# Optimization experiments

Hardware: AMD Instinct MI355X
Metric: run time of the kernel (lower is better)

## Reference

```python
import jax
import jax.numpy as jnp
import numpy as np

B, R, C, Q, D = 16, 2048, 81, 65, 1024
K = 1024          # pre-NMS candidate cap (fixed-shape stand-in for torch's dynamic filtering)
DET = 100         # detections_per_img
IMG = 640.0       # square image size (clip bound)
SCORE_THRESH = 0.05
NMS_THRESH = 0.5
MIN_SIZE = 0.01
BBOX_CLIP = float(np.log(1000.0 / 16.0))  # torchvision BoxCoder bbox_xform_clip
WX, WY, WW, WH = 10.0, 10.0, 5.0, 5.0     # BoxCoder weights


def setup_inputs() -> dict:
    key = jax.random.key(0)
    k1, k2, k3, k4, k5, k6 = jax.random.split(key, 6)
    class_logits = 2.0 * jax.random.normal(k1, (B, R, C), jnp.float32)
    quantity_logits = jax.random.normal(k2, (B, R, Q), jnp.float32)
    box_features = jax.random.normal(k3, (B, R, D), jnp.float32)
    box_regression = 0.5 * jax.random.normal(k4, (B, R, C * 4), jnp.float32)
    cxcy = jax.random.uniform(k5, (B, R, 2), jnp.float32, 0.0, IMG)
    wh = jax.random.uniform(k6, (B, R, 2), jnp.float32, 10.0, 80.0)
    x1y1 = jnp.clip(cxcy - 0.5 * wh, 0.0, IMG)
    x2y2 = jnp.clip(cxcy + 0.5 * wh, 0.0, IMG)
    proposals = jnp.concatenate([x1y1, x2y2], axis=-1)
    return {
        'class_logits': class_logits,
        'quantity_logits': quantity_logits,
        'box_features': box_features,
        'box_regression': box_regression,
        'proposals': proposals,
    }


def _decode(deltas, props):
    # deltas: [R, C, 4], props: [R, 4] -> boxes [R, C, 4] (torchvision BoxCoder.decode)
    pw = props[:, 2] - props[:, 0]
    ph = props[:, 3] - props[:, 1]
    pcx = props[:, 0] + 0.5 * pw
    pcy = props[:, 1] + 0.5 * ph
    dx = deltas[..., 0] / WX
    dy = deltas[..., 1] / WY
    dw = jnp.minimum(deltas[..., 2] / WW, BBOX_CLIP)
    dh = jnp.minimum(deltas[..., 3] / WH, BBOX_CLIP)
    cx = dx * pw[:, None] + pcx[:, None]
    cy = dy * ph[:, None] + pcy[:, None]
    w = jnp.exp(dw) * pw[:, None]
    h = jnp.exp(dh) * ph[:, None]
    return jnp.stack([cx - 0.5 * w, cy - 0.5 * h, cx + 0.5 * w, cy + 0.5 * h], axis=-1)


def _iou_matrix(b):
    # b: [K, 4] -> pairwise IoU [K, K]
    area = (b[:, 2] - b[:, 0]) * (b[:, 3] - b[:, 1])
    lt = jnp.maximum(b[:, None, :2], b[None, :, :2])
    rb = jnp.minimum(b[:, None, 2:], b[None, :, 2:])
    whv = jnp.clip(rb - lt, 0.0)
    inter = whv[..., 0] * whv[..., 1]
    return inter / (area[:, None] + area[None, :] - inter + 1e-9)


def _process_image(logits, qlogits, feats, reg, props):
    # decode + clip
    boxes = jnp.clip(_decode(reg.reshape(R, C, 4), props), 0.0, IMG)  # [R, C, 4]
    scores = jax.nn.softmax(logits, axis=-1)                          # [R, C]
    quant = jnp.argmax(qlogits, axis=-1).astype(jnp.int32)            # [R]
    # drop background class 0, flatten to M = R*(C-1)
    fb = boxes[:, 1:, :].reshape(-1, 4)
    fs = scores[:, 1:].reshape(-1)
    fl = jnp.broadcast_to(jnp.arange(1, C, dtype=jnp.int32), (R, C - 1)).reshape(-1)
    fi = jnp.broadcast_to(jnp.arange(R, dtype=jnp.int32)[:, None], (R, C - 1)).reshape(-1)
    bw = fb[:, 2] - fb[:, 0]
    bh = fb[:, 3] - fb[:, 1]
    valid = (fs > SCORE_THRESH) & (bw >= MIN_SIZE) & (bh >= MIN_SIZE)
    # top-K candidates by masked score (sorted desc)
    top_s, top_i = jax.lax.top_k(jnp.where(valid, fs, -1.0), K)
    cb = fb[top_i]          # [K, 4]
    cl = fl[top_i]          # [K]
    ci = fi[top_i]          # [K] row index into proposals/features
    cv = top_s > 0.0        # candidate validity (score_thresh > 0)
    # batched NMS via per-class coordinate offset
    ob = cb + (cl.astype(jnp.float32) * (IMG + 1.0))[:, None]
    iou = _iou_matrix(ob)
    ar = jnp.arange(K)

    def body(i, keep):
        sup = (iou[i] > NMS_THRESH) & (ar > i)
        return jnp.where(keep[i] & cv[i], keep & ~sup, keep)

    keep = jax.lax.fori_loop(0, K, body, cv) & cv
    # first DET survivors in score order
    det_s, det_i = jax.lax.top_k(jnp.where(keep, top_s, -1.0), DET)
    dv = det_s > 0.0
    m = dv.astype(jnp.float32)
    db = cb[det_i] * m[:, None]
    dl = jnp.where(dv, cl[det_i], 0)
    di = ci[det_i]
    dq = jnp.where(dv, quant[di], 0)
    df = feats[di] * m[:, None]   # irregular gather of box features by surviving row idx
    ds = jnp.where(dv, det_s, 0.0)
    return db, ds, dl, dq, df, dv


def reference(class_logits, quantity_logits, box_features, box_regression, proposals):
    # returns (boxes [B,DET,4], scores [B,DET], labels [B,DET] i32,
    #          quantities [B,DET] i32, features [B,DET,D], valid [B,DET] bool)
    return jax.vmap(_process_image)(class_logits, quantity_logits, box_features,
                                    box_regression, proposals)
```

## Files before the change

### kernel.cpp

```cpp
#include <hip/hip_runtime.h>
#include <math.h>

#define NB 16
#define NR 2048
#define NC 81
#define NQ 65
#define ND 1024
#define NK 1024
#define NDET 100
#define NBLK 512
#define BSLOT 64
#define HBINS 5184
#define BBC 4.135166556742356f

#define O_BOX   0
#define O_SCORE (NB*NDET*4)
#define O_LABEL (O_SCORE + NB*NDET)
#define O_QUANT (O_LABEL + NB*NDET)
#define O_FEAT  (O_QUANT + NB*NDET)
#define O_VALID (O_FEAT + (size_t)NB*NDET*ND)

#define WS_CAND  ((size_t)0)
#define WS_CNT   (WS_CAND + (size_t)NB*NBLK*BSLOT*8)
#define WS_QUANT (WS_CNT + (size_t)NB*NBLK*4)
#define WS_SELM  (WS_QUANT + (size_t)NB*NR*4)
#define WS_SELS  (WS_SELM + (size_t)NB*NK*4)
#define WS_CB    (WS_SELS + (size_t)NB*NK*4)
#define WS_DETK  (WS_CB + (size_t)NB*NK*16)

__device__ __forceinline__ float4 decode_box(float4 d, float pw, float ph,
                                             float pcx, float pcy) {
    float dx = d.x / 10.0f, dy = d.y / 10.0f;
    float dw = fminf(d.z / 5.0f, BBC), dh = fminf(d.w / 5.0f, BBC);
    float cx = dx * pw + pcx, cy = dy * ph + pcy;
    float w = expf(dw) * pw, h = expf(dh) * ph;
    float4 r;
    r.x = fminf(fmaxf(cx - 0.5f * w, 0.0f), 640.0f);
    r.y = fminf(fmaxf(cy - 0.5f * h, 0.0f), 640.0f);
    r.z = fminf(fmaxf(cx + 0.5f * w, 0.0f), 640.0f);
    r.w = fminf(fmaxf(cy + 0.5f * h, 0.0f), 640.0f);
    return r;
}

__global__ __launch_bounds__(256) void k_stage1(
    const float* __restrict__ logits, const float* __restrict__ qlog,
    const float* __restrict__ reg, const float* __restrict__ props,
    unsigned long long* __restrict__ cand, int* __restrict__ cnt,
    int* __restrict__ quant) {
    __shared__ unsigned long long sl[BSLOT];
    __shared__ int scnt;
    int b = blockIdx.x >> 9;
    int blk = blockIdx.x & (NBLK - 1);
    int wid = threadIdx.x >> 6;
    int lane = threadIdx.x & 63;
    int r = blk * 4 + wid;
    int row = b * NR + r;
    if (threadIdx.x == 0) scnt = 0;
    __syncthreads();

    const float* Lrow = logits + (size_t)row * NC;
    float v0 = Lrow[lane];
    float v1 = (lane < NC - 64) ? Lrow[64 + lane] : -1e30f;
    float mx = fmaxf(v0, v1);
    #pragma unroll
    for (int o = 32; o; o >>= 1) mx = fmaxf(mx, __shfl_xor(mx, o));
    float e = expf(v0 - mx) + ((lane < NC - 64) ? expf(v1 - mx) : 0.0f);
    float sm = e;
    #pragma unroll
    for (int o = 32; o; o >>= 1) sm += __shfl_xor(sm, o);
    float thr_lo = mx + logf(0.05f * sm) - 0.01f;

    const float* Qrow = qlog + (size_t)row * NQ;
    float qv = Qrow[lane];
    int qi = lane;
    if (lane == 0) {
        float q64 = Qrow[64];
        if (q64 > qv) { qv = q64; qi = 64; }
    }
    #pragma unroll
    for (int o = 32; o; o >>= 1) {
        float ov = __shfl_xor(qv, o);
        int oi = __shfl_xor(qi, o);
        if (ov > qv || (ov == qv && oi < qi)) { qv = ov; qi = oi; }
    }
    if (lane == 0) quant[row] = qi;

    const float* P = props + (size_t)row * 4;
    float p0 = P[0], p1 = P[1], p2 = P[2], p3 = P[3];
    float pw = p2 - p0, ph = p3 - p1;
    float pcx = p0 + 0.5f * pw, pcy = p1 + 0.5f * ph;
    const float* G = reg + (size_t)row * (NC * 4);

    #pragma unroll
    for (int pass = 0; pass < 2; ++pass) {
        int cc = lane + pass * 64;
        if (cc < NC - 1) {
            int c = cc + 1;
            float lc = Lrow[c];
            if (lc > thr_lo) {
                float p = expf(lc - mx) / sm;
                float4 d = *(const float4*)(G + 4 * c);
                float4 bx = decode_box(d, pw, ph, pcx, pcy);
                float bw = bx.z - bx.x, bh = bx.w - bx.y;
                if (p > 0.05f && bw >= 0.01f && bh >= 0.01f) {
                    int m = r * 80 + cc;
                    int pos = atomicAdd(&scnt, 1);
                    if (pos < BSLOT)
                        sl[pos] = ((unsigned long long)__float_as_uint(p) << 32) |
                                  (unsigned)(~(unsigned)m);
                }
            }
        }
    }
    __syncthreads();
    int n = scnt < BSLOT ? scnt : BSLOT;
    unsigned long long* dst = cand + ((size_t)b * NBLK + blk) * BSLOT;
    for (int i = threadIdx.x; i < n; i += 256) dst[i] = sl[i];
    if (threadIdx.x == 0) cnt[b * NBLK + blk] = n;
}

__global__ __launch_bounds__(1024) void k_fused(
    const unsigned long long* __restrict__ cand, const int* __restrict__ cnt,
    const float* __restrict__ reg, const float* __restrict__ props,
    int* __restrict__ sel_m, float* __restrict__ sel_s,
    float4* __restrict__ cb, int* __restrict__ det_k) {
    __shared__ unsigned int hist[HBINS];
    __shared__ unsigned long long list[2048];
    __shared__ float4 boxes[NK];
    __shared__ int scn[NBLK];
    __shared__ int s_cnt, s_bstar, s_n;
    int b = blockIdx.x, tid = threadIdx.x;
    const unsigned long long* cnd = cand + (size_t)b * NBLK * BSLOT;

    for (int i = tid; i < HBINS; i += 1024) hist[i] = 0;
    if (tid < NBLK) scn[tid] = cnt[b * NBLK + tid];
    if (tid == 0) { s_cnt = 0; s_bstar = 0; }
    __syncthreads();

    for (int i = tid; i < NBLK * BSLOT; i += 1024) {
        if ((i & (BSLOT - 1)) < scn[i >> 6]) {
            unsigned bits = (unsigned)(cnd[i] >> 32);
            atomicAdd(&hist[(bits - 0x3D000000u) >> 13], 1u);
        }
    }
    __syncthreads();

    if (tid < 64) {
        int lane = tid, base = lane * 81;
        unsigned partial = 0;
        for (int j = 0; j < 81; ++j) partial += hist[base + j];
        unsigned incl = partial;
        #pragma unroll
        for (int o = 1; o < 64; o <<= 1) {
            unsigned t = __shfl_up(incl, o);
            if (lane >= o) incl += t;
        }
        unsigned total = __shfl(incl, 63);
        unsigned suffix = total - incl;
        if (suffix < NK && suffix + partial >= NK) {
            unsigned A = suffix;
            int bcross = base;
            for (int bb = base + 80; bb >= base; --bb) {
                unsigned An = A + hist[bb];
                if (An >= NK) { bcross = bb; break; }
                A = An;
            }
            s_bstar = bcross;
        }
    }
    __syncthreads();
    int bstar = s_bstar;

    for (int i = tid; i < NBLK * BSLOT; i += 1024) {
        if ((i & (BSLOT - 1)) < scn[i >> 6]) {
            unsigned long long key = cnd[i];
            int bin = (int)(((unsigned)(key >> 32) - 0x3D000000u) >> 13);
            if (bin >= bstar) {
                int p = atomicAdd(&s_cnt, 1);
                if (p < 2048) list[p] = key;
            }
        }
    }
    __syncthreads();
    int S = s_cnt;
    if (S > 2048) S = 2048;
    int n = 2;
    while (n < S) n <<= 1;
    for (int i = S + tid; i < n; i += 1024) list[i] = 0ull;
    __syncthreads();

    for (int k2 = 2; k2 <= n; k2 <<= 1)
        for (int j = k2 >> 1; j > 0; j >>= 1) {
            for (int i = tid; i < n; i += 1024) {
                int ixj = i ^ j;
                if (ixj > i) {
                    unsigned long long a = list[i], c = list[ixj];
                    bool descRegion = ((i & k2) == 0);
                    if ((a < c) == descRegion) { list[i] = c; list[ixj] = a; }
                }
            }
            __syncthreads();
        }

    int L = S < NK ? S : NK;
    if (tid == 0) s_n = L;
    if (tid < L) {
        unsigned long long key = list[tid];
        int m = (int)(~(unsigned)key);
        sel_m[b * NK + tid] = m;
        sel_s[b * NK + tid] = __uint_as_float((unsigned)(key >> 32));
        int r = m / 80, c = m - r * 80 + 1;
        size_t row = (size_t)b * NR + r;
        const float* P = props + row * 4;
        float p0 = P[0], p1 = P[1], p2 = P[2], p3 = P[3];
        float pw = p2 - p0, ph = p3 - p1;
        float pcx = p0 + 0.5f * pw, pcy = p1 + 0.5f * ph;
        float4 d = *(const float4*)(reg + row * (NC * 4) + 4 * c);
        float4 bx = decode_box(d, pw, ph, pcx, pcy);
        cb[(size_t)b * NK + tid] = bx;
        float off = (float)c * 641.0f;
        float4 o = {bx.x + off, bx.y + off, bx.z + off, bx.w + off};
        boxes[tid] = o;
    }
    __syncthreads();

    if (tid < 64) {
        int lane = tid, nn = s_n, A = 0;
        float4 a0 = {0, 0, 0, 0}, a1 = {0, 0, 0, 0};
        int* dk = det_k + b * NDET;
        float4 nxt = (nn > 0) ? boxes[0] : a0;
        for (int t = 0; t < nn && A < NDET; ++t) {
            float4 bt = nxt;
            if (t + 1 < nn) nxt = boxes[t + 1];
            float areaB = (bt.z - bt.x) * (bt.w - bt.y);
            float areaA0 = (a0.z - a0.x) * (a0.w - a0.y);
            float ltx = fmaxf(a0.x, bt.x), lty = fmaxf(a0.y, bt.y);
            float rbx = fminf(a0.z, bt.z), rby = fminf(a0.w, bt.w);
            float inter = fmaxf(rbx - ltx, 0.0f) * fmaxf(rby - lty, 0.0f);
            bool sup = (lane < A) &&
                       (inter / (areaA0 + areaB - inter + 1e-9f) > 0.5f);
            if (A > 64) {
                float areaA1 = (a1.z - a1.x) * (a1.w - a1.y);
                float ltx1 = fmaxf(a1.x, bt.x), lty1 = fmaxf(a1.y, bt.y);
                float rbx1 = fminf(a1.z, bt.z), rby1 = fminf(a1.w, bt.w);
                float in1 = fmaxf(rbx1 - ltx1, 0.0f) * fmaxf(rby1 - lty1, 0.0f);
                sup |= (lane + 64 < A) &&
                       (in1 / (areaA1 + areaB - in1 + 1e-9f) > 0.5f);
            }
            if (!__any((int)sup)) {
                if (lane == (A & 63)) {
                    if (A < 64) a0 = bt; else a1 = bt;
                }
                if (lane == 0) dk[A] = t;
                ++A;
            }
        }
        for (int d = A + lane; d < NDET; d += 64) dk[d] = -1;
    }
}

__global__ __launch_bounds__(256) void k_final(
    const float* __restrict__ feats, const int* __restrict__ quant,
    const int* __restrict__ sel_m, const float* __restrict__ sel_s,
    const float4* __restrict__ cb, const int* __restrict__ det_k,
    float* __restrict__ out) {
    int bd = blockIdx.x;
    int b = bd / NDET, d = bd - b * NDET;
    int t = threadIdx.x;
    int k = det_k[b * NDET + d];
    float4* of = (float4*)(out + O_FEAT + (size_t)bd * ND);
    if (k >= 0) {
        int m = sel_m[b * NK + k];
        int r = m / 80, c = m - r * 80 + 1;
        if (t == 0) {
            ((float4*)(out + O_BOX))[bd] = cb[(size_t)b * NK + k];
            out[O_SCORE + bd] = sel_s[b * NK + k];
            out[O_LABEL + bd] = (float)c;
            out[O_QUANT + bd] = (float)quant[b * NR + r];
            out[O_VALID + bd] = 1.0f;
        }
        const float4* f = (const float4*)(feats + ((size_t)b * NR + r) * ND);
        of[t] = f[t];
    } else {
        if (t == 0) {
            float4 z = {0, 0, 0, 0};
            ((float4*)(out + O_BOX))[bd] = z;
            out[O_SCORE + bd] = 0.0f;
            out[O_LABEL + bd] = 0.0f;
            out[O_QUANT + bd] = 0.0f;
            out[O_VALID + bd] = 0.0f;
        }
        float4 z = {0, 0, 0, 0};
        of[t] = z;
    }
}

extern "C" void kernel_launch(void* const* d_in, const int* in_sizes, int n_in,
                              void* d_out, int out_size, void* d_ws, size_t ws_size,
                              hipStream_t stream) {
    const float* logits = (const float*)d_in[0];
    const float* qlog   = (const float*)d_in[1];
    const float* feats  = (const float*)d_in[2];
    const float* reg    = (const float*)d_in[3];
    const float* props  = (const float*)d_in[4];
    float* out = (float*)d_out;
    char* ws = (char*)d_ws;

    unsigned long long* cand = (unsigned long long*)(ws + WS_CAND);
    int* cnt = (int*)(ws + WS_CNT);
    int* quant = (int*)(ws + WS_QUANT);
    int* sel_m = (int*)(ws + WS_SELM);
    float* sel_s = (float*)(ws + WS_SELS);
    float4* cb = (float4*)(ws + WS_CB);
    int* det_k = (int*)(ws + WS_DETK);

    k_stage1<<<NB * NBLK, 256, 0, stream>>>(logits, qlog, reg, props, cand, cnt,
                                            quant);
    k_fused<<<NB, 1024, 0, stream>>>(cand, cnt, reg, props, sel_m, sel_s, cb,
                                     det_k);
    k_final<<<NB * NDET, 256, 0, stream>>>(feats, quant, sel_m, sel_s, cb, det_k,
                                           out);
}
```

Baseline: 304.7 us.

## Build histogram in stage1, two-tier rank sort, lazy NMS of tail candidates

The score histogram is now built with global atomics in stage1, so the single-block fused kernel no longer makes an extra pass over candidates. The top-1024 bitonic sort is replaced by a two-tier selection: the top ~256 candidates are rank-sorted and run through NMS first. The remaining candidates are only rank-sorted and decoded when fewer than 100 detections survive. The quantity argmax moves from all rows into the final kernel, which runs it only for surviving detections. The trade-offs are a memset plus global atomics, and an O(n^2) rank sort in the fallback path.

```diff
diff --git a/kernel.cpp b/kernel.cpp
--- a/kernel.cpp
+++ b/kernel.cpp
@@ -11,6 +11,9 @@
 #define NBLK 512
 #define BSLOT 64
 #define HBINS 5184
+#define CH 256
+#define L2CAP 384
+#define LRCAP 1536
 #define BBC 4.135166556742356f
 
 #define O_BOX   0
@@ -21,12 +24,11 @@
 #define O_VALID (O_FEAT + (size_t)NB*NDET*ND)
 
 #define WS_CAND  ((size_t)0)
-#define WS_CNT   (WS_CAND + (size_t)NB*NBLK*BSLOT*8)
-#define WS_QUANT (WS_CNT + (size_t)NB*NBLK*4)
-#define WS_SELM  (WS_QUANT + (size_t)NB*NR*4)
-#define WS_SELS  (WS_SELM + (size_t)NB*NK*4)
-#define WS_CB    (WS_SELS + (size_t)NB*NK*4)
-#define WS_DETK  (WS_CB + (size_t)NB*NK*16)
+#define WS_GHIST (WS_CAND + (size_t)NB*NBLK*BSLOT*8)
+#define WS_DETCB (WS_GHIST + (size_t)NB*HBINS*4)
+#define WS_DETM  (WS_DETCB + (size_t)NB*NDET*16)
+#define WS_DETS  (WS_DETM + (size_t)NB*NDET*4)
+#define WS_CNT   (WS_DETS + (size_t)NB*NDET*4)
 
 __device__ __forceinline__ float4 decode_box(float4 d, float pw, float ph,
                                              float pcx, float pcy) {
@@ -43,10 +45,9 @@
 }
 
 __global__ __launch_bounds__(256) void k_stage1(
-    const float* __restrict__ logits, const float* __restrict__ qlog,
-    const float* __restrict__ reg, const float* __restrict__ props,
-    unsigned long long* __restrict__ cand, int* __restrict__ cnt,
-    int* __restrict__ quant) {
+    const float* __restrict__ logits, const float* __restrict__ reg,
+    const float* __restrict__ props, unsigned long long* __restrict__ cand,
+    int* __restrict__ cnt, unsigned int* __restrict__ ghist) {
     __shared__ unsigned long long sl[BSLOT];
     __shared__ int scnt;
     int b = blockIdx.x >> 9;
@@ -69,21 +70,6 @@
     #pragma unroll
     for (int o = 32; o; o >>= 1) sm += __shfl_xor(sm, o);
     float thr_lo = mx + logf(0.05f * sm) - 0.01f;
-
-    const float* Qrow = qlog + (size_t)row * NQ;
-    float qv = Qrow[lane];
-    int qi = lane;
-    if (lane == 0) {
-        float q64 = Qrow[64];
-        if (q64 > qv) { qv = q64; qi = 64; }
-    }
-    #pragma unroll
-    for (int o = 32; o; o >>= 1) {
-        float ov = __shfl_xor(qv, o);
-        int oi = __shfl_xor(qi, o);
-        if (ov > qv || (ov == qv && oi < qi)) { qv = ov; qi = oi; }
-    }
-    if (lane == 0) quant[row] = qi;
 
     const float* P = props + (size_t)row * 4;
     float p0 = P[0], p1 = P[1], p2 = P[2], p3 = P[3];
@@ -105,9 +91,12 @@
                 if (p > 0.05f && bw >= 0.01f && bh >= 0.01f) {
                     int m = r * 80 + cc;
                     int pos = atomicAdd(&scnt, 1);
-                    if (pos < BSLOT)
+                    if (pos < BSLOT) {
                         sl[pos] = ((unsigned long long)__float_as_uint(p) << 32) |
                                   (unsigned)(~(unsigned)m);
+                        unsigned bin = (__float_as_uint(p) - 0x3D000000u) >> 13;
+                        atomicAdd(&ghist[b * HBINS + bin], 1u);
+                    }
                 }
             }
         }
@@ -121,34 +110,31 @@
 
 __global__ __launch_bounds__(1024) void k_fused(
     const unsigned long long* __restrict__ cand, const int* __restrict__ cnt,
+    const unsigned int* __restrict__ ghist,
     const float* __restrict__ reg, const float* __restrict__ props,
-    int* __restrict__ sel_m, float* __restrict__ sel_s,
-    float4* __restrict__ cb, int* __restrict__ det_k) {
-    __shared__ unsigned int hist[HBINS];
-    __shared__ unsigned long long list[2048];
-    __shared__ float4 boxes[NK];
+    int* __restrict__ det_m, float* __restrict__ det_s,
+    float4* __restrict__ det_cb) {
+    __shared__ union {
+        unsigned int hist[HBINS];
+        unsigned long long sortedRest[LRCAP];
+    } u;
+    __shared__ unsigned long long list2[L2CAP], sorted2[L2CAP];
+    __shared__ unsigned long long listRest[LRCAP];
+    __shared__ float4 boff[L2CAP], bclip[L2CAP];
     __shared__ int scn[NBLK];
-    __shared__ int s_cnt, s_bstar, s_n;
+    __shared__ int s_c2, s_cR, s_b1, s_b2, s_A, s_need;
     int b = blockIdx.x, tid = threadIdx.x;
     const unsigned long long* cnd = cand + (size_t)b * NBLK * BSLOT;
 
-    for (int i = tid; i < HBINS; i += 1024) hist[i] = 0;
+    for (int i = tid; i < HBINS; i += 1024) u.hist[i] = ghist[b * HBINS + i];
     if (tid < NBLK) scn[tid] = cnt[b * NBLK + tid];
-    if (tid == 0) { s_cnt = 0; s_bstar = 0; }
-    __syncthreads();
-
-    for (int i = tid; i < NBLK * BSLOT; i += 1024) {
-        if ((i & (BSLOT - 1)) < scn[i >> 6]) {
-            unsigned bits = (unsigned)(cnd[i] >> 32);
-            atomicAdd(&hist[(bits - 0x3D000000u) >> 13], 1u);
-        }
-    }
+    if (tid == 0) { s_c2 = 0; s_cR = 0; s_b1 = 0; s_b2 = 0; s_A = 0; s_need = 0; }
     __syncthreads();
 
     if (tid < 64) {
         int lane = tid, base = lane * 81;
         unsigned partial = 0;
-        for (int j = 0; j < 81; ++j) partial += hist[base + j];
+        for (int j = 0; j < 81; ++j) partial += u.hist[base + j];
         unsigned incl = partial;
         #pragma unroll
         for (int o = 1; o < 64; o <<= 1) {
@@ -159,127 +145,198 @@
         unsigned suffix = total - incl;
         if (suffix < NK && suffix + partial >= NK) {
             unsigned A = suffix;
-            int bcross = base;
             for (int bb = base + 80; bb >= base; --bb) {
-                unsigned An = A + hist[bb];
-                if (An >= NK) { bcross = bb; break; }
+                unsigned An = A + u.hist[bb];
+                if (An >= NK) { s_b1 = bb; break; }
                 A = An;
             }
-            s_bstar = bcross;
-        }
-    }
-    __syncthreads();
-    int bstar = s_bstar;
+        }
+        if (suffix < CH && suffix + partial >= CH) {
+            unsigned A = suffix;
+            for (int bb = base + 80; bb >= base; --bb) {
+                unsigned An = A + u.hist[bb];
+                if (An >= CH) { s_b2 = bb; break; }
+                A = An;
+            }
+        }
+    }
+    __syncthreads();
+    int b1 = s_b1, b2 = s_b2;
 
     for (int i = tid; i < NBLK * BSLOT; i += 1024) {
         if ((i & (BSLOT - 1)) < scn[i >> 6]) {
             unsigned long long key = cnd[i];
             int bin = (int)(((unsigned)(key >> 32) - 0x3D000000u) >> 13);
-            if (bin >= bstar) {
-                int p = atomicAdd(&s_cnt, 1);
-                if (p < 2048) list[p] = key;
-            }
-        }
-    }
-    __syncthreads();
-    int S = s_cnt;
-    if (S > 2048) S = 2048;
-    int n = 2;
-    while (n < S) n <<= 1;
-    for (int i = S + tid; i < n; i += 1024) list[i] = 0ull;
-    __syncthreads();
-
-    for (int k2 = 2; k2 <= n; k2 <<= 1)
-        for (int j = k2 >> 1; j > 0; j >>= 1) {
-            for (int i = tid; i < n; i += 1024) {
-                int ixj = i ^ j;
-                if (ixj > i) {
-                    unsigned long long a = list[i], c = list[ixj];
-                    bool descRegion = ((i & k2) == 0);
-                    if ((a < c) == descRegion) { list[i] = c; list[ixj] = a; }
-                }
-            }
-            __syncthreads();
-        }
-
-    int L = S < NK ? S : NK;
-    if (tid == 0) s_n = L;
-    if (tid < L) {
-        unsigned long long key = list[tid];
+            if (bin >= b2) {
+                int p = atomicAdd(&s_c2, 1);
+                if (p < L2CAP) list2[p] = key;
+            } else if (bin >= b1) {
+                int p = atomicAdd(&s_cR, 1);
+                if (p < LRCAP) listRest[p] = key;
+            }
+        }
+    }
+    __syncthreads();
+    int T2 = s_c2 < L2CAP ? s_c2 : L2CAP;
+    int TR = s_cR < LRCAP ? s_cR : LRCAP;
+    int S = T2 + TR;
+    int cap = S < NK ? S : NK;
+    int limit1 = T2 < cap ? T2 : cap;
+
+    if (tid < T2) {
+        unsigned long long k0 = list2[tid];
+        int rk = 0;
+        for (int j = 0; j < T2; ++j) rk += (list2[j] > k0);
+        sorted2[rk] = k0;
+    }
+    __syncthreads();
+
+    if (tid < limit1) {
+        unsigned long long key = sorted2[tid];
         int m = (int)(~(unsigned)key);
-        sel_m[b * NK + tid] = m;
-        sel_s[b * NK + tid] = __uint_as_float((unsigned)(key >> 32));
         int r = m / 80, c = m - r * 80 + 1;
         size_t row = (size_t)b * NR + r;
-        const float* P = props + row * 4;
-        float p0 = P[0], p1 = P[1], p2 = P[2], p3 = P[3];
-        float pw = p2 - p0, ph = p3 - p1;
-        float pcx = p0 + 0.5f * pw, pcy = p1 + 0.5f * ph;
+        float4 P = *(const float4*)(props + row * 4);
+        float pw = P.z - P.x, ph = P.w - P.y;
+        float pcx = P.x + 0.5f * pw, pcy = P.y + 0.5f * ph;
         float4 d = *(const float4*)(reg + row * (NC * 4) + 4 * c);
         float4 bx = decode_box(d, pw, ph, pcx, pcy);
-        cb[(size_t)b * NK + tid] = bx;
+        bclip[tid] = bx;
         float off = (float)c * 641.0f;
         float4 o = {bx.x + off, bx.y + off, bx.z + off, bx.w + off};
-        boxes[tid] = o;
-    }
-    __syncthreads();
-
+        boff[tid] = o;
+    }
+    __syncthreads();
+
+    int lane = tid & 63;
+    float4 a0 = {0, 0, 0, 0}, a1 = {0, 0, 0, 0};
+    int A = 0;
     if (tid < 64) {
-        int lane = tid, nn = s_n, A = 0;
-        float4 a0 = {0, 0, 0, 0}, a1 = {0, 0, 0, 0};
-        int* dk = det_k + b * NDET;
-        float4 nxt = (nn > 0) ? boxes[0] : a0;
-        for (int t = 0; t < nn && A < NDET; ++t) {
-            float4 bt = nxt;
-            if (t + 1 < nn) nxt = boxes[t + 1];
+        unsigned long long nk_ = (limit1 > 0) ? sorted2[0] : 0ull;
+        float4 nb_ = (limit1 > 0) ? boff[0] : a0;
+        for (int t = 0; t < limit1; ++t) {
+            unsigned long long keyt = nk_;
+            float4 bt = nb_;
+            if (t + 1 < limit1) { nk_ = sorted2[t + 1]; nb_ = boff[t + 1]; }
             float areaB = (bt.z - bt.x) * (bt.w - bt.y);
             float areaA0 = (a0.z - a0.x) * (a0.w - a0.y);
             float ltx = fmaxf(a0.x, bt.x), lty = fmaxf(a0.y, bt.y);
             float rbx = fminf(a0.z, bt.z), rby = fminf(a0.w, bt.w);
-            float inter = fmaxf(rbx - ltx, 0.0f) * fmaxf(rby - lty, 0.0f);
-            bool sup = (lane < A) &&
-                       (inter / (areaA0 + areaB - inter + 1e-9f) > 0.5f);
+            float in0 = fmaxf(rbx - ltx, 0.0f) * fmaxf(rby - lty, 0.0f);
+            bool sup = (lane < A) && (in0 / (areaA0 + areaB - in0 + 1e-9f) > 0.5f);
             if (A > 64) {
                 float areaA1 = (a1.z - a1.x) * (a1.w - a1.y);
-                float ltx1 = fmaxf(a1.x, bt.x), lty1 = fmaxf(a1.y, bt.y);
-                float rbx1 = fminf(a1.z, bt.z), rby1 = fminf(a1.w, bt.w);
-                float in1 = fmaxf(rbx1 - ltx1, 0.0f) * fmaxf(rby1 - lty1, 0.0f);
+                float l1 = fmaxf(a1.x, bt.x), t1 = fmaxf(a1.y, bt.y);
+                float r1 = fminf(a1.z, bt.z), b1f = fminf(a1.w, bt.w);
+                float in1 = fmaxf(r1 - l1, 0.0f) * fmaxf(b1f - t1, 0.0f);
                 sup |= (lane + 64 < A) &&
                        (in1 / (areaA1 + areaB - in1 + 1e-9f) > 0.5f);
             }
             if (!__any((int)sup)) {
-                if (lane == (A & 63)) {
-                    if (A < 64) a0 = bt; else a1 = bt;
+                if (lane == (A & 63)) { if (A < 64) a0 = bt; else a1 = bt; }
+                if (lane == 0) {
+                    det_m[b * NDET + A] = (int)(~(unsigned)keyt);
+                    det_s[b * NDET + A] = __uint_as_float((unsigned)(keyt >> 32));
+                    det_cb[b * NDET + A] = bclip[t];
                 }
-                if (lane == 0) dk[A] = t;
                 ++A;
-            }
-        }
-        for (int d = A + lane; d < NDET; d += 64) dk[d] = -1;
-    }
+                if (A == NDET) break;
+            }
+        }
+        if (tid == 0) { s_A = A; s_need = (A < NDET && limit1 < cap) ? 1 : 0; }
+    }
+    __syncthreads();
+
+    if (s_need) {
+        for (int t0 = tid; t0 < TR; t0 += 1024) {
+            unsigned long long k0 = listRest[t0];
+            int rk = 0;
+            for (int j = 0; j < TR; ++j) rk += (listRest[j] > k0);
+            u.sortedRest[rk] = k0;
+        }
+        __syncthreads();
+        if (tid < 64) {
+            int nrest = cap - limit1;
+            for (int t = 0; t < nrest && A < NDET; ++t) {
+                unsigned long long keyt = u.sortedRest[t];
+                int m = (int)(~(unsigned)keyt);
+                int r = m / 80, c = m - r * 80 + 1;
+                size_t row = (size_t)b * NR + r;
+                float4 P = *(const float4*)(props + row * 4);
+                float pw = P.z - P.x, ph = P.w - P.y;
+                float pcx = P.x + 0.5f * pw, pcy = P.y + 0.5f * ph;
+                float4 d = *(const float4*)(reg + row * (NC * 4) + 4 * c);
+                float4 bx = decode_box(d, pw, ph, pcx, pcy);
+                float off = (float)c * 641.0f;
+                float4 bt = {bx.x + off, bx.y + off, bx.z + off, bx.w + off};
+                float areaB = (bt.z - bt.x) * (bt.w - bt.y);
+                float areaA0 = (a0.z - a0.x) * (a0.w - a0.y);
+                float ltx = fmaxf(a0.x, bt.x), lty = fmaxf(a0.y, bt.y);
+                float rbx = fminf(a0.z, bt.z), rby = fminf(a0.w, bt.w);
+                float in0 = fmaxf(rbx - ltx, 0.0f) * fmaxf(rby - lty, 0.0f);
+                bool sup = (lane < A) &&
+                           (in0 / (areaA0 + areaB - in0 + 1e-9f) > 0.5f);
+                if (A > 64) {
+                    float areaA1 = (a1.z - a1.x) * (a1.w - a1.y);
+                    float l1 = fmaxf(a1.x, bt.x), t1 = fmaxf(a1.y, bt.y);
+                    float r1 = fminf(a1.z, bt.z), b1f = fminf(a1.w, bt.w);
+                    float in1 = fmaxf(r1 - l1, 0.0f) * fmaxf(b1f - t1, 0.0f);
+                    sup |= (lane + 64 < A) &&
+                           (in1 / (areaA1 + areaB - in1 + 1e-9f) > 0.5f);
+                }
+                if (!__any((int)sup)) {
+                    if (lane == (A & 63)) { if (A < 64) a0 = bt; else a1 = bt; }
+                    if (lane == 0) {
+                        det_m[b * NDET + A] = m;
+                        det_s[b * NDET + A] =
+                            __uint_as_float((unsigned)(keyt >> 32));
+                        det_cb[b * NDET + A] = bx;
+                    }
+                    ++A;
+                }
+            }
+            if (tid == 0) s_A = A;
+        }
+        __syncthreads();
+    }
+    for (int d = s_A + tid; d < NDET; d += 1024) det_m[b * NDET + d] = -1;
 }
 
 __global__ __launch_bounds__(256) void k_final(
-    const float* __restrict__ feats, const int* __restrict__ quant,
-    const int* __restrict__ sel_m, const float* __restrict__ sel_s,
-    const float4* __restrict__ cb, const int* __restrict__ det_k,
-    float* __restrict__ out) {
+    const float* __restrict__ feats, const float* __restrict__ qlog,
+    const int* __restrict__ det_m, const float* __restrict__ det_s,
+    const float4* __restrict__ det_cb, float* __restrict__ out) {
     int bd = blockIdx.x;
-    int b = bd / NDET, d = bd - b * NDET;
+    int b = bd / NDET;
     int t = threadIdx.x;
-    int k = det_k[b * NDET + d];
+    int m = det_m[bd];
     float4* of = (float4*)(out + O_FEAT + (size_t)bd * ND);
-    if (k >= 0) {
-        int m = sel_m[b * NK + k];
+    if (m >= 0) {
         int r = m / 80, c = m - r * 80 + 1;
+        size_t row = (size_t)b * NR + r;
         if (t == 0) {
-            ((float4*)(out + O_BOX))[bd] = cb[(size_t)b * NK + k];
-            out[O_SCORE + bd] = sel_s[b * NK + k];
+            ((float4*)(out + O_BOX))[bd] = det_cb[bd];
+            out[O_SCORE + bd] = det_s[bd];
             out[O_LABEL + bd] = (float)c;
-            out[O_QUANT + bd] = (float)quant[b * NR + r];
             out[O_VALID + bd] = 1.0f;
         }
-        const float4* f = (const float4*)(feats + ((size_t)b * NR + r) * ND);
+        if (t < 64) {
+            const float* Qrow = qlog + row * NQ;
+            float qv = Qrow[t];
+            int qi = t;
+            if (t == 0) {
+                float q64 = Qrow[64];
+                if (q64 > qv) { qv = q64; qi = 64; }
+            }
+            #pragma unroll
+            for (int o = 32; o; o >>= 1) {
+                float ov = __shfl_xor(qv, o);
+                int oi = __shfl_xor(qi, o);
+                if (ov > qv || (ov == qv && oi < qi)) { qv = ov; qi = oi; }
+            }
+            if (t == 0) out[O_QUANT + bd] = (float)qi;
+        }
+        const float4* f = (const float4*)(feats + row * ND);
         of[t] = f[t];
     } else {
         if (t == 0) {
@@ -307,17 +364,15 @@
     char* ws = (char*)d_ws;
 
     unsigned long long* cand = (unsigned long long*)(ws + WS_CAND);
+    unsigned int* ghist = (unsigned int*)(ws + WS_GHIST);
+    float4* det_cb = (float4*)(ws + WS_DETCB);
+    int* det_m = (int*)(ws + WS_DETM);
+    float* det_s = (float*)(ws + WS_DETS);
     int* cnt = (int*)(ws + WS_CNT);
-    int* quant = (int*)(ws + WS_QUANT);
-    int* sel_m = (int*)(ws + WS_SELM);
-    float* sel_s = (float*)(ws + WS_SELS);
-    float4* cb = (float4*)(ws + WS_CB);
-    int* det_k = (int*)(ws + WS_DETK);
-
-    k_stage1<<<NB * NBLK, 256, 0, stream>>>(logits, qlog, reg, props, cand, cnt,
-                                            quant);
-    k_fused<<<NB, 1024, 0, stream>>>(cand, cnt, reg, props, sel_m, sel_s, cb,
-                                     det_k);
-    k_final<<<NB * NDET, 256, 0, stream>>>(feats, quant, sel_m, sel_s, cb, det_k,
-                                           out);
-}
+
+    hipMemsetAsync(ghist, 0, (size_t)NB * HBINS * 4, stream);
+    k_stage1<<<NB * NBLK, 256, 0, stream>>>(logits, reg, props, cand, cnt, ghist);
+    k_fused<<<NB, 1024, 0, stream>>>(cand, cnt, ghist, reg, props, det_m, det_s,
+                                     det_cb);
+    k_final<<<NB * NDET, 256, 0, stream>>>(feats, qlog, det_m, det_s, det_cb, out);
+}
```

Result: faster. 294.8 us (-3.2%).
